# Kernel optimization log

Hardware: AMD Instinct MI355X
Metric: run time of the kernel (lower is better)

## Reference

```python
import jax, jax.numpy as jnp
import numpy as np

G, N, E, F_IN, F_OUT, C = 256, 512, 4096, 64, 64, 16


def setup_inputs() -> dict:
    key = jax.random.key(0)
    ks = jax.random.split(key, 6)
    x_batch = jax.random.normal(ks[0], (G, N, F_IN), dtype=jnp.float32)
    edge_index_batch = jax.random.randint(ks[1], (G, 2, E), 0, N, dtype=jnp.int32)
    conv_weight = jax.random.normal(ks[2], (F_OUT, F_IN), dtype=jnp.float32) * (1.0 / np.sqrt(F_IN))
    conv_bias = jax.random.normal(ks[3], (F_OUT,), dtype=jnp.float32) * 0.02
    lin_weight = jax.random.normal(ks[4], (C, F_OUT * N), dtype=jnp.float32) * (1.0 / np.sqrt(F_OUT * N))
    lin_bias = jax.random.normal(ks[5], (C,), dtype=jnp.float32) * 0.02
    return {"x_batch": x_batch, "edge_index_batch": edge_index_batch,
            "conv_weight": conv_weight, "conv_bias": conv_bias,
            "lin_weight": lin_weight, "lin_bias": lin_bias}


def _gcn_conv_graph(xw, edge_index, self_loops):
    # xw: [N, F_OUT] (already linearly transformed), edge_index: [2, E]
    row = jnp.concatenate([edge_index[0], self_loops])  # sources
    col = jnp.concatenate([edge_index[1], self_loops])  # targets
    ones = jnp.ones(row.shape[0], dtype=xw.dtype)
    deg = jax.ops.segment_sum(ones, col, num_segments=N)  # degree at target nodes
    dinv = jnp.where(deg > 0, jax.lax.rsqrt(deg), jnp.zeros_like(deg))
    norm = dinv[row] * dinv[col]                          # [E+N]
    msgs = xw[row] * norm[:, None]                        # gather + normalize
    return jax.ops.segment_sum(msgs, col, num_segments=N)  # scatter-add at targets


def reference(x_batch, edge_index_batch, conv_weight, conv_bias, lin_weight, lin_bias):
    # GCNConv (PyG defaults: self-loops, symmetric normalization, post-agg bias)
    xw = jnp.einsum('gnf,of->gno', x_batch, conv_weight)  # [G, N, F_OUT]
    self_loops = jnp.arange(N, dtype=edge_index_batch.dtype)
    h = jax.vmap(_gcn_conv_graph, in_axes=(0, 0, None))(xw, edge_index_batch, self_loops)
    h = h + conv_bias
    h = jax.nn.relu(h)
    flat = h.reshape(h.shape[0], -1)                      # [G, N*F_OUT]
    logits = flat @ lin_weight.T + lin_bias               # [G, C]
    return jax.nn.log_softmax(logits, axis=-1)
```

## Files before the change

### kernel.cpp

```cpp
#include <hip/hip_runtime.h>

#define Gn 256
#define Nn 512
#define En 4096
#define Fn 64
#define Cn 16
#define ET (En + Nn)

typedef _Float16 halfv8 __attribute__((ext_vector_type(8)));
typedef _Float16 halfv4 __attribute__((ext_vector_type(4)));
typedef float    f32x4  __attribute__((ext_vector_type(4)));

__device__ __forceinline__ float pk_norm(unsigned p) {
    return (float)__builtin_bit_cast(_Float16, (unsigned short)(p & 0xffffu));
}

__global__ __launch_bounds__(1024, 4) void gcn_agg_conv(
    const float* __restrict__ x,
    const int*   __restrict__ ei,
    const float* __restrict__ w,
    const float* __restrict__ wbias,
    _Float16* __restrict__ hout)
{
    __shared__ unsigned short xs_h[Nn * Fn];
    __shared__ unsigned short xhs[Nn * Fn];
    __shared__ unsigned short wts[Fn * Fn];
    __shared__ unsigned int   epk[ET + 8];
    __shared__ float dinv[Nn];
    __shared__ int   cnt[Nn];
    __shared__ int   wsum[8];

    const int g    = blockIdx.x;
    const int tid  = threadIdx.x;
    const int lane = tid & 63;
    const int wid  = tid >> 6;

    const float* xg = x + (size_t)g * Nn * Fn;
    const int*   es = ei + (size_t)g * 2 * En;
    const int*   ed = es + En;

    if (tid < Nn) dinv[tid] = 1.0f;
    __syncthreads();

    for (int e = tid; e < En; e += 1024) atomicAdd(&dinv[ed[e]], 1.0f);
    #pragma unroll
    for (int it = 0; it < 8; ++it) {
        int idx = tid + it * 1024;
        float4 v = *(const float4*)(xg + idx * 4);
        halfv4 hv; hv[0]=(_Float16)v.x; hv[1]=(_Float16)v.y;
                   hv[2]=(_Float16)v.z; hv[3]=(_Float16)v.w;
        *(halfv4*)((char*)xs_h + idx * 8) = hv;
    }
    {
        int o = tid >> 4, f0 = (tid & 15) * 4;
        float4 v = *(const float4*)(w + o * Fn + f0);
        halfv4 hv; hv[0]=(_Float16)v.x; hv[1]=(_Float16)v.y;
                   hv[2]=(_Float16)v.z; hv[3]=(_Float16)v.w;
        int blk = f0 >> 3, hf = (f0 >> 2) & 1;
        *(halfv4*)((char*)wts + o * 128 + ((blk ^ (o & 7)) * 16) + hf * 8) = hv;
    }
    __syncthreads();

    int c = 0;
    if (tid < Nn) { float d = dinv[tid]; c = (int)d; dinv[tid] = rsqrtf(d); }
    int v_ = c;
    #pragma unroll
    for (int off = 1; off < 64; off <<= 1) {
        int u = __shfl_up(v_, off, 64);
        if (lane >= off) v_ += u;
    }
    if (wid < 8 && lane == 63) wsum[wid] = v_;
    __syncthreads();
    if (tid == 0) { int a = 0; for (int i = 0; i < 8; ++i) { int t = wsum[i]; wsum[i] = a; a += t; } }
    __syncthreads();
    if (tid < Nn) cnt[tid] = v_ - c + wsum[wid];
    __syncthreads();

    for (int e = tid; e < ET; e += 1024) {
        int s, t;
        if (e < En) { s = es[e]; t = ed[e]; } else { s = e - En; t = s; }
        float nrm = dinv[s] * dinv[t];
        int slot = atomicAdd(&cnt[t], 1);
        unsigned short nb = __builtin_bit_cast(unsigned short, (_Float16)nrm);
        epk[slot] = ((unsigned)s << 16) | nb;
    }
    __syncthreads();

    {
        const int qid = lane >> 4, fl = lane & 15;
        for (int r = 0; r < 8; ++r) {
            int t = r * 64 + wid * 4 + qid;
            int beg = (t == 0) ? 0 : cnt[t - 1];
            int end = cnt[t];
            float a0 = 0.f, a1 = 0.f, a2 = 0.f, a3 = 0.f;
            unsigned pA0 = epk[beg],     pA1 = epk[beg + 1];
            unsigned pA2 = epk[beg + 2], pA3 = epk[beg + 3];
            int j = beg;
            for (; j + 4 <= end; j += 4) {
                unsigned pB0 = epk[j + 4], pB1 = epk[j + 5];
                unsigned pB2 = epk[j + 6], pB3 = epk[j + 7];
                int s0 = pA0 >> 16, s1 = pA1 >> 16, s2 = pA2 >> 16, s3 = pA3 >> 16;
                float n0 = pk_norm(pA0), n1 = pk_norm(pA1);
                float n2 = pk_norm(pA2), n3 = pk_norm(pA3);
                halfv4 x0 = *(const halfv4*)((const char*)xs_h + s0 * 128 + fl * 8);
                halfv4 x1 = *(const halfv4*)((const char*)xs_h + s1 * 128 + fl * 8);
                halfv4 x2 = *(const halfv4*)((const char*)xs_h + s2 * 128 + fl * 8);
                halfv4 x3 = *(const halfv4*)((const char*)xs_h + s3 * 128 + fl * 8);
                a0 += n0 * (float)x0[0] + n1 * (float)x1[0] + n2 * (float)x2[0] + n3 * (float)x3[0];
                a1 += n0 * (float)x0[1] + n1 * (float)x1[1] + n2 * (float)x2[1] + n3 * (float)x3[1];
                a2 += n0 * (float)x0[2] + n1 * (float)x1[2] + n2 * (float)x2[2] + n3 * (float)x3[2];
                a3 += n0 * (float)x0[3] + n1 * (float)x1[3] + n2 * (float)x2[3] + n3 * (float)x3[3];
                pA0 = pB0; pA1 = pB1; pA2 = pB2; pA3 = pB3;
            }
            for (; j < end; ++j) {
                int s = pA0 >> 16;
                float nm = pk_norm(pA0);
                halfv4 xv = *(const halfv4*)((const char*)xs_h + s * 128 + fl * 8);
                a0 += nm * (float)xv[0]; a1 += nm * (float)xv[1];
                a2 += nm * (float)xv[2]; a3 += nm * (float)xv[3];
                pA0 = pA1; pA1 = pA2; pA2 = pA3;
            }
            halfv4 hv; hv[0]=(_Float16)a0; hv[1]=(_Float16)a1;
                       hv[2]=(_Float16)a2; hv[3]=(_Float16)a3;
            int dw = t * 32 + (((fl >> 1) ^ (t & 7)) * 4) + (fl & 1) * 2;
            *(halfv4*)((char*)xhs + dw * 4) = hv;
        }
    }
    __syncthreads();

    {
        const int m = lane & 15, q = lane >> 4;
        #pragma unroll
        for (int j = 0; j < 8; ++j) {
            int idx = wid * 8 + j, tm = idx >> 2, to = idx & 3;
            int n = tm * 16 + m, o = to * 16 + m;
            halfv8 X0 = *(const halfv8*)((const char*)xhs + n * 128 + ((q       ^ (n & 7)) * 16));
            halfv8 X1 = *(const halfv8*)((const char*)xhs + n * 128 + (((4 + q) ^ (n & 7)) * 16));
            halfv8 W0 = *(const halfv8*)((const char*)wts + o * 128 + ((q       ^ (o & 7)) * 16));
            halfv8 W1 = *(const halfv8*)((const char*)wts + o * 128 + (((4 + q) ^ (o & 7)) * 16));
            f32x4 acc = {0.f, 0.f, 0.f, 0.f};
            acc = __builtin_amdgcn_mfma_f32_16x16x32_f16(W0, X0, acc, 0, 0, 0);
            acc = __builtin_amdgcn_mfma_f32_16x16x32_f16(W1, X1, acc, 0, 0, 0);
            float4 bq = *(const float4*)&wbias[to * 16 + q * 4];
            halfv4 hv;
            hv[0] = (_Float16)fmaxf(acc[0] + bq.x, 0.0f);
            hv[1] = (_Float16)fmaxf(acc[1] + bq.y, 0.0f);
            hv[2] = (_Float16)fmaxf(acc[2] + bq.z, 0.0f);
            hv[3] = (_Float16)fmaxf(acc[3] + bq.w, 0.0f);
            int sw = (to * 4 + q) ^ m;
            *(halfv4*)((char*)xs_h + n * 128 + sw * 8) = hv;
        }
    }
    __syncthreads();

    {
        _Float16* hg = hout + (size_t)g * (Nn * Fn);
        #pragma unroll
        for (int it = 0; it < 8; ++it) {
            int i = tid + it * 1024;
            int n = i >> 4, g64 = i & 15;
            uint2 vv = *(const uint2*)((const char*)xs_h + (n * 16 + (g64 ^ (n & 15))) * 8);
            *(uint2*)((char*)hg + (size_t)i * 8) = vv;
        }
    }
}

__global__ __launch_bounds__(256) void gcn_linear(
    const _Float16* __restrict__ h,
    const float* __restrict__ lw,
    float* __restrict__ part)
{
    __shared__ float red[4][64][4];
    const int cx = blockIdx.x;
    const int gy = blockIdx.y;
    const int tid = threadIdx.x, lane = tid & 63, wid = tid >> 6;
    const int ml = lane & 15, q = lane >> 4;

    const size_t kbase = (size_t)cx * 1024 + wid * 256;
    const _Float16* ha = h  + (size_t)(gy * 16 + ml) * (Nn * Fn) + kbase + q * 8;
    const float*    lb = lw + (size_t)ml * (Nn * Fn) + kbase + q * 8;

    f32x4 acc = {0.f, 0.f, 0.f, 0.f};
    #pragma unroll
    for (int ks = 0; ks < 8; ++ks) {
        halfv8 a = *(const halfv8*)(ha + ks * 32);
        float4 b0 = *(const float4*)(lb + ks * 32);
        float4 b1 = *(const float4*)(lb + ks * 32 + 4);
        halfv8 b; b[0]=(_Float16)b0.x; b[1]=(_Float16)b0.y; b[2]=(_Float16)b0.z;
                  b[3]=(_Float16)b0.w; b[4]=(_Float16)b1.x; b[5]=(_Float16)b1.y;
                  b[6]=(_Float16)b1.z; b[7]=(_Float16)b1.w;
        acc = __builtin_amdgcn_mfma_f32_16x16x32_f16(a, b, acc, 0, 0, 0);
    }
    #pragma unroll
    for (int r = 0; r < 4; ++r) red[wid][lane][r] = acc[r];
    __syncthreads();
    {
        int m = tid >> 4, cc = tid & 15;
        int sl = (m >> 2) * 16 + cc, rg = m & 3;
        float v = red[0][sl][rg] + red[1][sl][rg] + red[2][sl][rg] + red[3][sl][rg];
        part[(((size_t)(gy * 16 + m)) * 32 + cx) * Cn + cc] = v;
    }
}

__global__ __launch_bounds__(64) void gcn_softmax(
    const float* __restrict__ part,
    const float* __restrict__ lbias,
    float* __restrict__ out)
{
    const int g = blockIdx.x, lane = threadIdx.x;
    if (lane < Cn) {
        float v = lbias[lane];
        #pragma unroll
        for (int s = 0; s < 32; ++s) v += part[((size_t)g * 32 + s) * Cn + lane];
        float m = v;
        #pragma unroll
        for (int off = 8; off > 0; off >>= 1) m = fmaxf(m, __shfl_xor(m, off, 16));
        float ex = expf(v - m);
        float ssum = ex;
        #pragma unroll
        for (int off = 8; off > 0; off >>= 1) ssum += __shfl_xor(ssum, off, 16);
        out[g * Cn + lane] = v - m - logf(ssum);
    }
}

extern "C" void kernel_launch(void* const* d_in, const int* in_sizes, int n_in,
                              void* d_out, int out_size, void* d_ws, size_t ws_size,
                              hipStream_t stream) {
    const float* x  = (const float*)d_in[0];
    const int*   ei = (const int*)d_in[1];
    const float* w  = (const float*)d_in[2];
    const float* wb = (const float*)d_in[3];
    const float* lw = (const float*)d_in[4];
    const float* lb = (const float*)d_in[5];
    float* out = (float*)d_out;

    _Float16* hbuf = (_Float16*)d_ws;
    float* part = (float*)((char*)d_ws + (size_t)Gn * Nn * Fn * 2);

    hipLaunchKernelGGL(gcn_agg_conv, dim3(Gn), dim3(1024), 0, stream,
                       x, ei, w, wb, hbuf);
    hipLaunchKernelGGL(gcn_linear, dim3(32, 16), dim3(256), 0, stream,
                       hbuf, lw, part);
    hipLaunchKernelGGL(gcn_softmax, dim3(Gn), dim3(64), 0, stream,
                       part, lb, out);
}
```

Baseline: 115.7 us.

## Prefetch edge and feature loads into registers; pre-convert linear weights to fp16

```diff
diff --git a/kernel.cpp b/kernel.cpp
--- a/kernel.cpp
+++ b/kernel.cpp
@@ -9,6 +9,7 @@
 
 typedef _Float16 halfv8 __attribute__((ext_vector_type(8)));
 typedef _Float16 halfv4 __attribute__((ext_vector_type(4)));
+typedef _Float16 halfv2 __attribute__((ext_vector_type(2)));
 typedef float    f32x4  __attribute__((ext_vector_type(4)));
 
 __device__ __forceinline__ float pk_norm(unsigned p) {
@@ -20,7 +21,9 @@
     const int*   __restrict__ ei,
     const float* __restrict__ w,
     const float* __restrict__ wbias,
-    _Float16* __restrict__ hout)
+    const float* __restrict__ lw,
+    _Float16* __restrict__ hout,
+    _Float16* __restrict__ lwh)
 {
     __shared__ unsigned short xs_h[Nn * Fn];
     __shared__ unsigned short xhs[Nn * Fn];
@@ -39,50 +42,82 @@
     const int*   es = ei + (size_t)g * 2 * En;
     const int*   ed = es + En;
 
+    const int e0s = es[tid], e1s = es[tid + 1024], e2s = es[tid + 2048], e3s = es[tid + 3072];
+    const int e0t = ed[tid], e1t = ed[tid + 1024], e2t = ed[tid + 2048], e3t = ed[tid + 3072];
+    const float2 lv = *(const float2*)(lw + g * 2048 + tid * 2);
+    const float4 wv = *(const float4*)(w + (tid >> 4) * Fn + (tid & 15) * 4);
+    const int qq = (tid & 63) >> 4;
+    float4 bv[4];
+    #pragma unroll
+    for (int to = 0; to < 4; ++to) bv[to] = *(const float4*)&wbias[to * 16 + qq * 4];
+    float4 xv[8];
+    #pragma unroll
+    for (int it = 0; it < 8; ++it) xv[it] = *(const float4*)(xg + (tid + it * 1024) * 4);
+
     if (tid < Nn) dinv[tid] = 1.0f;
     __syncthreads();
 
-    for (int e = tid; e < En; e += 1024) atomicAdd(&dinv[ed[e]], 1.0f);
+    atomicAdd(&dinv[e0t], 1.0f);
+    atomicAdd(&dinv[e1t], 1.0f);
+    atomicAdd(&dinv[e2t], 1.0f);
+    atomicAdd(&dinv[e3t], 1.0f);
+    __syncthreads();
+
+    int c = 0;
+    if (tid < Nn) { float d = dinv[tid]; c = (int)d; dinv[tid] = rsqrtf(d); }
+    int v_ = c;
+    #pragma unroll
+    for (int off = 1; off < 64; off <<= 1) {
+        int u = __shfl_up(v_, off, 64);
+        if (lane >= off) v_ += u;
+    }
+    if (wid < 8 && lane == 63) wsum[wid] = v_;
+    __syncthreads();
+    if (tid == 0) { int a = 0; for (int i = 0; i < 8; ++i) { int t = wsum[i]; wsum[i] = a; a += t; } }
+    __syncthreads();
+    if (tid < Nn) cnt[tid] = v_ - c + wsum[wid];
+    __syncthreads();
+
+    {
+        #define FILL_EDGE(ss, tt) { \
+            float nrm = dinv[ss] * dinv[tt]; \
+            int slot = atomicAdd(&cnt[tt], 1); \
+            unsigned short nb = __builtin_bit_cast(unsigned short, (_Float16)nrm); \
+            epk[slot] = ((unsigned)(ss) << 16) | nb; }
+        FILL_EDGE(e0s, e0t)
+        FILL_EDGE(e1s, e1t)
+        FILL_EDGE(e2s, e2t)
+        FILL_EDGE(e3s, e3t)
+        #undef FILL_EDGE
+        if (tid < Nn) {
+            float dv = dinv[tid];
+            float nrm = dv * dv;
+            int slot = atomicAdd(&cnt[tid], 1);
+            unsigned short nb = __builtin_bit_cast(unsigned short, (_Float16)nrm);
+            epk[slot] = ((unsigned)tid << 16) | nb;
+        }
+    }
+
+    {
+        halfv2 hl; hl[0] = (_Float16)lv.x; hl[1] = (_Float16)lv.y;
+        *(halfv2*)(lwh + (size_t)g * 2048 + tid * 2) = hl;
+    }
+
+    {
+        int o = tid >> 4, f0 = (tid & 15) * 4;
+        halfv4 hv; hv[0]=(_Float16)wv.x; hv[1]=(_Float16)wv.y;
+                   hv[2]=(_Float16)wv.z; hv[3]=(_Float16)wv.w;
+        int blk = f0 >> 3, hf = (f0 >> 2) & 1;
+        *(halfv4*)((char*)wts + o * 128 + ((blk ^ (o & 7)) * 16) + hf * 8) = hv;
+    }
+
     #pragma unroll
     for (int it = 0; it < 8; ++it) {
         int idx = tid + it * 1024;
-        float4 v = *(const float4*)(xg + idx * 4);
+        float4 v = xv[it];
         halfv4 hv; hv[0]=(_Float16)v.x; hv[1]=(_Float16)v.y;
                    hv[2]=(_Float16)v.z; hv[3]=(_Float16)v.w;
         *(halfv4*)((char*)xs_h + idx * 8) = hv;
-    }
-    {
-        int o = tid >> 4, f0 = (tid & 15) * 4;
-        float4 v = *(const float4*)(w + o * Fn + f0);
-        halfv4 hv; hv[0]=(_Float16)v.x; hv[1]=(_Float16)v.y;
-                   hv[2]=(_Float16)v.z; hv[3]=(_Float16)v.w;
-        int blk = f0 >> 3, hf = (f0 >> 2) & 1;
-        *(halfv4*)((char*)wts + o * 128 + ((blk ^ (o & 7)) * 16) + hf * 8) = hv;
-    }
-    __syncthreads();
-
-    int c = 0;
-    if (tid < Nn) { float d = dinv[tid]; c = (int)d; dinv[tid] = rsqrtf(d); }
-    int v_ = c;
-    #pragma unroll
-    for (int off = 1; off < 64; off <<= 1) {
-        int u = __shfl_up(v_, off, 64);
-        if (lane >= off) v_ += u;
-    }
-    if (wid < 8 && lane == 63) wsum[wid] = v_;
-    __syncthreads();
-    if (tid == 0) { int a = 0; for (int i = 0; i < 8; ++i) { int t = wsum[i]; wsum[i] = a; a += t; } }
-    __syncthreads();
-    if (tid < Nn) cnt[tid] = v_ - c + wsum[wid];
-    __syncthreads();
-
-    for (int e = tid; e < ET; e += 1024) {
-        int s, t;
-        if (e < En) { s = es[e]; t = ed[e]; } else { s = e - En; t = s; }
-        float nrm = dinv[s] * dinv[t];
-        int slot = atomicAdd(&cnt[t], 1);
-        unsigned short nb = __builtin_bit_cast(unsigned short, (_Float16)nrm);
-        epk[slot] = ((unsigned)s << 16) | nb;
     }
     __syncthreads();
 
@@ -115,9 +150,9 @@
             for (; j < end; ++j) {
                 int s = pA0 >> 16;
                 float nm = pk_norm(pA0);
-                halfv4 xv = *(const halfv4*)((const char*)xs_h + s * 128 + fl * 8);
-                a0 += nm * (float)xv[0]; a1 += nm * (float)xv[1];
-                a2 += nm * (float)xv[2]; a3 += nm * (float)xv[3];
+                halfv4 xvv = *(const halfv4*)((const char*)xs_h + s * 128 + fl * 8);
+                a0 += nm * (float)xvv[0]; a1 += nm * (float)xvv[1];
+                a2 += nm * (float)xvv[2]; a3 += nm * (float)xvv[3];
                 pA0 = pA1; pA1 = pA2; pA2 = pA3;
             }
             halfv4 hv; hv[0]=(_Float16)a0; hv[1]=(_Float16)a1;
@@ -141,7 +176,7 @@
             f32x4 acc = {0.f, 0.f, 0.f, 0.f};
             acc = __builtin_amdgcn_mfma_f32_16x16x32_f16(W0, X0, acc, 0, 0, 0);
             acc = __builtin_amdgcn_mfma_f32_16x16x32_f16(W1, X1, acc, 0, 0, 0);
-            float4 bq = *(const float4*)&wbias[to * 16 + q * 4];
+            float4 bq = bv[j & 3];
             halfv4 hv;
             hv[0] = (_Float16)fmaxf(acc[0] + bq.x, 0.0f);
             hv[1] = (_Float16)fmaxf(acc[1] + bq.y, 0.0f);
@@ -167,7 +202,7 @@
 
 __global__ __launch_bounds__(256) void gcn_linear(
     const _Float16* __restrict__ h,
-    const float* __restrict__ lw,
+    const _Float16* __restrict__ lwh,
     float* __restrict__ part)
 {
     __shared__ float red[4][64][4];
@@ -177,18 +212,14 @@
     const int ml = lane & 15, q = lane >> 4;
 
     const size_t kbase = (size_t)cx * 1024 + wid * 256;
-    const _Float16* ha = h  + (size_t)(gy * 16 + ml) * (Nn * Fn) + kbase + q * 8;
-    const float*    lb = lw + (size_t)ml * (Nn * Fn) + kbase + q * 8;
+    const _Float16* ha = h   + (size_t)(gy * 16 + ml) * (Nn * Fn) + kbase + q * 8;
+    const _Float16* lb = lwh + (size_t)ml * (Nn * Fn) + kbase + q * 8;
 
     f32x4 acc = {0.f, 0.f, 0.f, 0.f};
     #pragma unroll
     for (int ks = 0; ks < 8; ++ks) {
         halfv8 a = *(const halfv8*)(ha + ks * 32);
-        float4 b0 = *(const float4*)(lb + ks * 32);
-        float4 b1 = *(const float4*)(lb + ks * 32 + 4);
-        halfv8 b; b[0]=(_Float16)b0.x; b[1]=(_Float16)b0.y; b[2]=(_Float16)b0.z;
-                  b[3]=(_Float16)b0.w; b[4]=(_Float16)b1.x; b[5]=(_Float16)b1.y;
-                  b[6]=(_Float16)b1.z; b[7]=(_Float16)b1.w;
+        halfv8 b = *(const halfv8*)(lb + ks * 32);
         acc = __builtin_amdgcn_mfma_f32_16x16x32_f16(a, b, acc, 0, 0, 0);
     }
     #pragma unroll
@@ -236,11 +267,13 @@
 
     _Float16* hbuf = (_Float16*)d_ws;
     float* part = (float*)((char*)d_ws + (size_t)Gn * Nn * Fn * 2);
+    _Float16* lwh = (_Float16*)((char*)d_ws + (size_t)Gn * Nn * Fn * 2
+                                            + (size_t)Gn * 32 * Cn * 4);
 
     hipLaunchKernelGGL(gcn_agg_conv, dim3(Gn), dim3(1024), 0, stream,
-                       x, ei, w, wb, hbuf);
+                       x, ei, w, wb, lw, hbuf, lwh);
     hipLaunchKernelGGL(gcn_linear, dim3(32, 16), dim3(256), 0, stream,
-                       hbuf, lw, part);
+                       hbuf, lwh, part);
     hipLaunchKernelGGL(gcn_softmax, dim3(Gn), dim3(64), 0, stream,
                        part, lb, out);
 }
```

After: 115.0 us. Within noise of the previous version (-0.6%).
